# Performance work log

Measured on AMD Instinct MI355X. Metric: run time of the kernel, lower is better.

Reference implementation:

```python
import jax, jax.numpy as jnp
import numpy as np

N_NODES, IN_DIM, HID, LAT, N_EDGES = 50000, 3000, 512, 30, 800000
NEG_SLOPE = 0.2


def setup_inputs() -> dict:
    key = jax.random.key(0)
    ks = jax.random.split(key, 6)
    x = jax.random.normal(ks[0], (N_NODES, IN_DIM), dtype=jnp.float32)
    edge_index = jax.random.randint(ks[1], (2, N_EDGES), 0, N_NODES, dtype=jnp.int64)
    # xavier-normal-ish scales
    W1 = jax.random.normal(ks[2], (IN_DIM, HID), dtype=jnp.float32) * 0.02
    W2 = jax.random.normal(ks[3], (HID, LAT), dtype=jnp.float32) * 0.06
    att_src = jax.random.normal(ks[4], (HID,), dtype=jnp.float32) * 0.1
    att_dst = jax.random.normal(ks[5], (HID,), dtype=jnp.float32) * 0.1
    return {"x": x, "edge_index": edge_index, "W1": W1, "W2": W2,
            "att_src": att_src, "att_dst": att_dst}


def _segment_softmax(e, seg, num_segments):
    # numerically stable softmax over variable-degree dst neighborhoods
    m = jax.ops.segment_max(e, seg, num_segments=num_segments)
    m = jnp.where(jnp.isfinite(m), m, 0.0)  # empty segments -> 0, harmless
    p = jnp.exp(e - m[seg])
    s = jax.ops.segment_sum(p, seg, num_segments=num_segments)
    return p / (s[seg] + 1e-16)


def reference(x, edge_index, W1, W2, att_src, att_dst):
    N = x.shape[0]
    src, dst = edge_index[0], edge_index[1]  # messages flow src(j) -> dst(i)

    # ---- conv1: full GAT layer (heads=1, no self-loops, no bias) ----
    h1 = x @ W1                                   # [N, 512]
    a_src = h1 @ att_src                          # [N]
    a_dst = h1 @ att_dst                          # [N]
    e = jax.nn.leaky_relu(a_src[src] + a_dst[dst], NEG_SLOPE)  # [E]
    alpha = _segment_softmax(e, dst, N)           # [E] (also tied attn for conv3)
    agg1 = jax.ops.segment_sum(h1[src] * alpha[:, None], dst, num_segments=N)
    x1 = jax.nn.elu(agg1)                         # [N, 512]

    # ---- conv2: attention=False -> plain linear projection ----
    x2 = x1 @ W2                                  # [N, 30] (latent embedding)

    # ---- conv3: tied weights (W2^T) + tied attention from conv1 ----
    h3 = x2 @ W2.T                                # [N, 512]
    agg3 = jax.ops.segment_sum(h3[src] * alpha[:, None], dst, num_segments=N)
    x3 = jax.nn.elu(agg3)

    # ---- conv4: attention=False, tied weights (W1^T) ----
    x4 = x3 @ W1.T                                # [N, in_channels]
    return (x2, x4)
```

## Files before the change

kernel.cpp:

```cpp
#include <hip/hip_runtime.h>

#define N_NODES 50000
#define IN_DIM  3000
#define HID     512
#define LAT     30
#define N_EDGES 800000
#define M_PAD   50048
#define K1_PAD  3008
#define N4_PAD  3072

typedef __bf16 bf16;
typedef unsigned int uint;
typedef __attribute__((ext_vector_type(4))) float f32x4;
typedef __attribute__((ext_vector_type(8))) bf16 bf16x8;

__device__ __forceinline__ float bf2f(bf16 b){ return (float)b; }

__device__ __forceinline__ void gl16(const void* g, void* l){
  __builtin_amdgcn_global_load_lds(
      (const __attribute__((address_space(1))) void*)g,
      (__attribute__((address_space(3))) void*)l, 16, 0, 0);
}

__device__ __forceinline__ int xcd_swz(int orig, int nwg){
  int q = nwg >> 3, r = nwg & 7;
  int xcd = orig & 7, lid = orig >> 3;
  return (xcd < r ? xcd*(q+1) : r*(q+1) + (xcd-r)*q) + lid;
}

__global__ void k_w1t(const float* __restrict__ W1, bf16* __restrict__ W1T){
  int k = blockIdx.x*256 + threadIdx.x;
  int n = blockIdx.y;
  if (k >= K1_PAD) return;
  float v = (k < IN_DIM) ? W1[(long)k*HID + n] : 0.f;
  W1T[(long)n*K1_PAD + k] = (bf16)v;
}
__global__ void k_w1p(const float* __restrict__ W1, bf16* __restrict__ W1P){
  int k = blockIdx.x*256 + threadIdx.x;
  int n = blockIdx.y;
  if (k >= HID) return;
  float v = (n < IN_DIM) ? W1[(long)n*HID + k] : 0.f;
  W1P[(long)n*HID + k] = (bf16)v;
}
__global__ void k_w2t(const float* __restrict__ W2, bf16* __restrict__ W2T){
  int k = blockIdx.x*256 + threadIdx.x;
  int n = blockIdx.y;
  if (k >= HID) return;
  float v = (n < LAT) ? W2[(long)k*LAT + n] : 0.f;
  W2T[(long)n*HID + k] = (bf16)v;
}
__global__ void k_w2p(const float* __restrict__ W2, bf16* __restrict__ W2P){
  int t = blockIdx.x*256 + threadIdx.x;
  if (t >= HID*32) return;
  int n = t >> 5, k = t & 31;
  W2P[t] = (bf16)((k < LAT) ? W2[(long)n*LAT + k] : 0.f);
}

__global__ __launch_bounds__(256) void gemm_a32(
    const float* __restrict__ X, const bf16* __restrict__ Bw, bf16* __restrict__ C)
{
  __shared__ bf16 Alds[2][128*32];
  __shared__ bf16 Blds[2][128*32];
  const int NBX = HID/128;
  const int tid  = threadIdx.x;
  const int lane = tid & 63;
  const int w    = tid >> 6;
  const int wm   = (w >> 1) * 64, wn = (w & 1) * 64;
  const int wgid = xcd_swz(blockIdx.x, gridDim.x);
  const int col0 = (wgid % NBX) * 128, row0 = (wgid / NBX) * 128;
  const int Ksteps = K1_PAD/32;

  f32x4 acc[4][4];
  #pragma unroll
  for (int mi=0;mi<4;mi++)
    #pragma unroll
    for (int ni=0;ni<4;ni++)
      acc[mi][ni] = (f32x4){0.f,0.f,0.f,0.f};

  const int arow = tid >> 1;
  const int cg   = (tid & 1) * 16;
  const float* pA = X + (long)min(row0 + arow, N_NODES-1) * IN_DIM;

  const int sr = tid >> 2;
  const int sc = (tid & 3) * 16;
  const char* gB = (const char*)(Bw + (long)(col0 + sr) * K1_PAD) + sc;
  const long bstep = (long)64 * K1_PAD * 2;
  char* lB0 = (char*)&Blds[0][0] + sr*64 + sc;
  char* lB1 = (char*)&Blds[1][0] + sr*64 + sc;

  {
    int kb = cg;
    float4 q0 = *(const float4*)(pA + kb);
    float4 q1 = *(const float4*)(pA + kb + 4);
    float4 q2 = *(const float4*)(pA + kb + 8);
    float4 q3 = *(const float4*)(pA + kb + 12);
    gl16(gB, lB0);
    gl16(gB + bstep, lB0 + 64*64);
    bf16x8 v0, v1;
    v0[0]=(bf16)q0.x; v0[1]=(bf16)q0.y; v0[2]=(bf16)q0.z; v0[3]=(bf16)q0.w;
    v0[4]=(bf16)q1.x; v0[5]=(bf16)q1.y; v0[6]=(bf16)q1.z; v0[7]=(bf16)q1.w;
    v1[0]=(bf16)q2.x; v1[1]=(bf16)q2.y; v1[2]=(bf16)q2.z; v1[3]=(bf16)q2.w;
    v1[4]=(bf16)q3.x; v1[5]=(bf16)q3.y; v1[6]=(bf16)q3.z; v1[7]=(bf16)q3.w;
    *(bf16x8*)&Alds[0][arow*32 + cg]     = v0;
    *(bf16x8*)&Alds[0][arow*32 + cg + 8] = v1;
  }

  for (int ks = 0; ks < Ksteps; ks++){
    const int c = ks & 1;
    __syncthreads();
    const bool pf = (ks+1 < Ksteps);
    float4 q0,q1,q2,q3;
    if (pf){
      int kb = (ks+1)*32 + cg;
      q0 = *(const float4*)(pA + min(kb,      IN_DIM-4));
      q1 = *(const float4*)(pA + min(kb + 4,  IN_DIM-4));
      q2 = *(const float4*)(pA + min(kb + 8,  IN_DIM-4));
      q3 = *(const float4*)(pA + min(kb + 12, IN_DIM-4));
      const char* g = gB + (long)(ks+1)*64;
      char* l = c ? lB0 : lB1;
      gl16(g, l);
      gl16(g + bstep, l + 64*64);
    }
    bf16x8 af[4], bfr[4];
    #pragma unroll
    for (int mi=0;mi<4;mi++)
      af[mi] = *(const bf16x8*)&Alds[c][(wm + mi*16 + (lane & 15))*32 + (lane>>4)*8];
    #pragma unroll
    for (int ni=0;ni<4;ni++)
      bfr[ni] = *(const bf16x8*)&Blds[c][(wn + ni*16 + (lane & 15))*32 + (lane>>4)*8];
    #pragma unroll
    for (int mi=0;mi<4;mi++)
      #pragma unroll
      for (int ni=0;ni<4;ni++)
        acc[mi][ni] = __builtin_amdgcn_mfma_f32_16x16x32_bf16(af[mi], bfr[ni], acc[mi][ni], 0, 0, 0);
    if (pf){
      bf16x8 v0, v1;
      v0[0]=(bf16)q0.x; v0[1]=(bf16)q0.y; v0[2]=(bf16)q0.z; v0[3]=(bf16)q0.w;
      v0[4]=(bf16)q1.x; v0[5]=(bf16)q1.y; v0[6]=(bf16)q1.z; v0[7]=(bf16)q1.w;
      v1[0]=(bf16)q2.x; v1[1]=(bf16)q2.y; v1[2]=(bf16)q2.z; v1[3]=(bf16)q2.w;
      v1[4]=(bf16)q3.x; v1[5]=(bf16)q3.y; v1[6]=(bf16)q3.z; v1[7]=(bf16)q3.w;
      *(bf16x8*)&Alds[c^1][arow*32 + cg]     = v0;
      *(bf16x8*)&Alds[c^1][arow*32 + cg + 8] = v1;
    }
  }

  const int crb  = (lane >> 4) * 4;
  const int ccol = lane & 15;
  #pragma unroll
  for (int mi=0;mi<4;mi++){
    #pragma unroll
    for (int v=0;v<4;v++){
      int r = row0 + wm + mi*16 + crb + v;
      if (r >= N_NODES) continue;
      #pragma unroll
      for (int ni=0;ni<4;ni++){
        int cc = col0 + wn + ni*16 + ccol;
        C[(long)r*HID + cc] = (bf16)acc[mi][ni][v];
      }
    }
  }
}

template<bool C_F32, bool ELU>
__global__ __launch_bounds__(256) void gemm_glds(
    const bf16* __restrict__ A, const bf16* __restrict__ B, void* __restrict__ Cp,
    int lda, int ldb, int Ksteps, int Mvalid, int Nvalid, int ldc, int NBX)
{
  __shared__ bf16 Alds[128*32];
  __shared__ bf16 Blds[128*32];
  const int tid  = threadIdx.x;
  const int lane = tid & 63;
  const int w    = tid >> 6;
  const int wm   = (w >> 1) * 64, wn = (w & 1) * 64;
  const int wgid = xcd_swz(blockIdx.x, gridDim.x);
  const int col0 = (wgid % NBX) * 128, row0 = (wgid / NBX) * 128;

  f32x4 acc[4][4];
  #pragma unroll
  for (int mi=0;mi<4;mi++)
    #pragma unroll
    for (int ni=0;ni<4;ni++)
      acc[mi][ni] = (f32x4){0.f,0.f,0.f,0.f};

  const int sr = tid >> 2;
  const int sc = (tid & 3) * 16;

  const char* ga = (const char*)(A + (long)(row0 + sr) * lda) + sc;
  const char* gb = (const char*)(B + (long)(col0 + sr) * ldb) + sc;
  char* la = (char*)Alds + sr*64 + sc;
  char* lb = (char*)Blds + sr*64 + sc;
  const long astep = (long)64 * lda * 2;
  const long bstep = (long)64 * ldb * 2;

  for (int ks = 0; ks < Ksteps; ks++){
    const long ko = (long)ks * 64;
    gl16(ga + ko,         la);
    gl16(ga + ko + astep, la + 64*64);
    gl16(gb + ko,         lb);
    gl16(gb + ko + bstep, lb + 64*64);
    __syncthreads();

    bf16x8 af[4], bfr[4];
    #pragma unroll
    for (int mi=0;mi<4;mi++)
      af[mi] = *(const bf16x8*)&Alds[(wm + mi*16 + (lane & 15))*32 + (lane>>4)*8];
    #pragma unroll
    for (int ni=0;ni<4;ni++)
      bfr[ni] = *(const bf16x8*)&Blds[(wn + ni*16 + (lane & 15))*32 + (lane>>4)*8];
    #pragma unroll
    for (int mi=0;mi<4;mi++)
      #pragma unroll
      for (int ni=0;ni<4;ni++)
        acc[mi][ni] = __builtin_amdgcn_mfma_f32_16x16x32_bf16(af[mi], bfr[ni], acc[mi][ni], 0, 0, 0);
    __syncthreads();
  }

  const int crb  = (lane >> 4) * 4;
  const int ccol = lane & 15;
  #pragma unroll
  for (int mi=0;mi<4;mi++){
    #pragma unroll
    for (int v=0;v<4;v++){
      int r = row0 + wm + mi*16 + crb + v;
      if (r >= Mvalid) continue;
      #pragma unroll
      for (int ni=0;ni<4;ni++){
        int c = col0 + wn + ni*16 + ccol;
        if (c >= Nvalid) continue;
        float val = acc[mi][ni][v];
        if (ELU) val = (val > 0.f) ? val : expm1f(val);
        if (C_F32) ((float*)Cp)[(long)r*ldc + c] = val;
        else       ((bf16*)Cp)[(long)r*ldc + c] = (bf16)val;
      }
    }
  }
}

__global__ void k_attdots(const bf16* __restrict__ h1, const float* __restrict__ att_s,
                          const float* __restrict__ att_d, float* __restrict__ a_src,
                          float* __restrict__ a_dst){
  int gid = blockIdx.x * blockDim.x + threadIdx.x;
  int row = gid >> 6, lane = gid & 63;
  if (row >= N_NODES) return;
  bf16x8 hv = *(const bf16x8*)(h1 + (long)row*HID + lane*8);
  float s1 = 0.f, s2 = 0.f;
  #pragma unroll
  for (int j=0;j<8;j++){
    float h = bf2f(hv[j]);
    s1 = fmaf(h, att_s[lane*8+j], s1);
    s2 = fmaf(h, att_d[lane*8+j], s2);
  }
  #pragma unroll
  for (int o=32;o>0;o>>=1){ s1 += __shfl_down(s1,o); s2 += __shfl_down(s2,o); }
  if (lane == 0){ a_src[row] = s1; a_dst[row] = s2; }
}

__global__ void k_deg(const int* __restrict__ ei, int* __restrict__ deg){
  int e = blockIdx.x*256 + threadIdx.x;
  if (e >= N_EDGES) return;
  atomicAdd(&deg[ei[N_EDGES + e]], 1);
}

__global__ void k_scan(const int* __restrict__ deg, int* __restrict__ off, int* __restrict__ cur){
  const int n = M_PAD, T = 1024;
  int t = threadIdx.x;
  const int per = (n + T - 1) / T;
  int s0 = t*per, s1 = min(n, s0+per);
  int sum = 0;
  for (int i=s0;i<s1;i++) sum += deg[i];
  __shared__ int sd[1024];
  sd[t] = sum; __syncthreads();
  for (int o=1;o<T;o<<=1){
    int x = (t>=o) ? sd[t-o] : 0;
    __syncthreads();
    sd[t] += x;
    __syncthreads();
  }
  int run = sd[t] - sum;
  for (int i=s0;i<s1;i++){
    off[i] = run; cur[i] = run;
    run += deg[i];
  }
  if (s0 < n && s1 == n) off[n] = run;
}

__global__ void k_fill(const int* __restrict__ ei, int* __restrict__ cur,
                       int* __restrict__ csr_src, const float* __restrict__ a_s,
                       const float* __restrict__ a_d, float* __restrict__ p_e){
  int e = blockIdx.x*256 + threadIdx.x;
  if (e >= N_EDGES) return;
  int s = ei[e];
  int d = ei[N_EDGES + e];
  int pos = atomicAdd(&cur[d], 1);
  csr_src[pos] = s;
  float v = a_s[s] + a_d[d];
  v = (v > 0.f) ? v : 0.2f*v;
  p_e[pos] = __expf(v);
}

__global__ __launch_bounds__(512) void k_agg1(
    const int* __restrict__ off, const int* __restrict__ csr_src,
    const float* __restrict__ p_edge,
    const bf16* __restrict__ h1, bf16* __restrict__ x1,
    float* __restrict__ s_node)
{
  const int i = blockIdx.x;
  const int t = threadIdx.x;
  const int start = off[i];
  const int deg = off[i+1] - start;
  __shared__ float p_sh[512];
  __shared__ int   s_sh[512];

  float acc = 0.f, ssum = 0.f;
  for (int base=0; base<deg; base+=512){
    int cnt = min(512, deg-base);
    if (t < cnt){
      p_sh[t] = p_edge[start+base+t];
      s_sh[t] = csr_src[start+base+t];
    }
    __syncthreads();
    for (int k=0;k<cnt;k++){
      float pk = p_sh[k];
      ssum += pk;
      acc = fmaf(pk, bf2f(h1[(long)s_sh[k]*HID + t]), acc);
    }
    __syncthreads();
  }
  float val = acc / (ssum + 1e-16f);
  val = (val > 0.f) ? val : expm1f(val);
  x1[(long)i*HID + t] = (bf16)val;
  if (t == 0) s_node[i] = ssum;
}

__global__ void k_agg3(const int* __restrict__ off, const int* __restrict__ csr_src,
                       const float* __restrict__ p_edge, const float* __restrict__ s_node,
                       const float* __restrict__ x2, bf16* __restrict__ aggb)
{
  int i = blockIdx.x*8 + (threadIdx.x >> 5);
  int lane = threadIdx.x & 31;
  if (i >= M_PAD) return;
  float acc = 0.f;
  if (i < N_NODES){
    int s0 = off[i], d = off[i+1] - s0;
    for (int k=0;k<d;k++){
      int s = csr_src[s0+k];
      float pk = p_edge[s0+k];
      if (lane < LAT) acc = fmaf(pk, x2[(long)s*LAT + lane], acc);
    }
    acc *= 1.f/(s_node[i] + 1e-16f);
  }
  aggb[(long)i*32 + lane] = (bf16)((lane < LAT) ? acc : 0.f);
}

extern "C" void kernel_launch(void* const* d_in, const int* in_sizes, int n_in,
                              void* d_out, int out_size, void* d_ws, size_t ws_size,
                              hipStream_t stream)
{
  const float* x     = (const float*)d_in[0];
  const int*   ei    = (const int*)d_in[1];
  const float* W1    = (const float*)d_in[2];
  const float* W2    = (const float*)d_in[3];
  const float* att_s = (const float*)d_in[4];
  const float* att_d = (const float*)d_in[5];

  float* out_x2 = (float*)d_out;
  float* out_x4 = (float*)d_out + (long)N_NODES*LAT;

  bf16* h1 = (bf16*)out_x4;
  bf16* x1 = h1 + (long)M_PAD*HID;

  char* w = (char*)d_ws;
  bf16* W1T = (bf16*)w;  w += (long)HID*K1_PAD*2;
  bf16* W1P = (bf16*)w;  w += (long)N4_PAD*HID*2;
  bf16* W2T = (bf16*)w;  w += (long)128*HID*2;
  bf16* W2P = (bf16*)w;  w += (long)HID*32*2;
  bf16* x3  = (bf16*)w;  w += (long)M_PAD*HID*2;
  bf16* aggb= (bf16*)w;  w += (long)M_PAD*32*2;
  int* deg  = (int*)w;   w += (long)M_PAD*4;
  int* offs = (int*)w;   w += (long)(M_PAD+64)*4;
  int* cur  = (int*)w;   w += (long)M_PAD*4;
  int* csr  = (int*)w;   w += (long)N_EDGES*4;
  float* p_e = (float*)w; w += (long)N_EDGES*4;
  float* s_n = (float*)w; w += (long)M_PAD*4;
  float* a_s = (float*)w; w += (long)M_PAD*4;
  float* a_d = (float*)w; w += (long)M_PAD*4;

  k_w1t<<<dim3((K1_PAD+255)/256, HID), 256, 0, stream>>>(W1, W1T);
  k_w1p<<<dim3((HID+255)/256, N4_PAD), 256, 0, stream>>>(W1, W1P);
  k_w2t<<<dim3(2, 128), 256, 0, stream>>>(W2, W2T);
  k_w2p<<<(HID*32+255)/256, 256, 0, stream>>>(W2, W2P);

  hipMemsetAsync(deg, 0, (size_t)M_PAD*4, stream);
  k_deg<<<(N_EDGES+255)/256, 256, 0, stream>>>(ei, deg);
  k_scan<<<1, 1024, 0, stream>>>(deg, offs, cur);

  gemm_a32<<<(M_PAD/128)*(HID/128), 256, 0, stream>>>(x, W1T, h1);

  k_attdots<<<(N_NODES*64)/256, 256, 0, stream>>>(h1, att_s, att_d, a_s, a_d);

  k_fill<<<(N_EDGES+255)/256, 256, 0, stream>>>(ei, cur, csr, a_s, a_d, p_e);

  k_agg1<<<N_NODES, 512, 0, stream>>>(offs, csr, p_e, h1, x1, s_n);

  gemm_glds<true,false><<<1*(M_PAD/128), 256, 0, stream>>>(
      x1, W2T, out_x2, HID, HID, HID/32, N_NODES, LAT, LAT, 1);

  k_agg3<<<(M_PAD+7)/8, 256, 0, stream>>>(offs, csr, p_e, s_n, out_x2, aggb);
  gemm_glds<false,true><<<(HID/128)*(M_PAD/128), 256, 0, stream>>>(
      aggb, W2P, x3, 32, 32, 1, M_PAD, HID, HID, HID/128);

  gemm_glds<true,false><<<(N4_PAD/128)*(M_PAD/128), 256, 0, stream>>>(
      x3, W1P, out_x4, HID, HID, HID/32, N_NODES, IN_DIM, IN_DIM, N4_PAD/128);
}
```

Measured before the change: 1.362 ms.

## Load GEMM A operand directly into MFMA registers, dropping LDS staging for X

The first GEMM (x @ W1) now has each lane load its fp32 X fragments from global memory straight into registers in MFMA layout and convert to bf16 in place, instead of staging A through LDS. B still goes through double-buffered global_load_lds, with manual vmcnt waits and barriers, in a two-deep register/LDS pipeline unrolled by two. The aim is to remove LDS traffic and a sync for A and to keep more loads in flight. The cost is uncoalesced, strided 32-byte row reads of X duplicated across the two column-half waves, plus higher register pressure under launch_bounds(256,2).

```diff
diff --git a/kernel.cpp b/kernel.cpp
--- a/kernel.cpp
+++ b/kernel.cpp
@@ -28,6 +28,13 @@
   return (xcd < r ? xcd*(q+1) : r*(q+1) + (xcd-r)*q) + lid;
 }
 
+__device__ __forceinline__ bf16x8 cvt8(float4 a, float4 b){
+  bf16x8 r;
+  r[0]=(bf16)a.x; r[1]=(bf16)a.y; r[2]=(bf16)a.z; r[3]=(bf16)a.w;
+  r[4]=(bf16)b.x; r[5]=(bf16)b.y; r[6]=(bf16)b.z; r[7]=(bf16)b.w;
+  return r;
+}
+
 __global__ void k_w1t(const float* __restrict__ W1, bf16* __restrict__ W1T){
   int k = blockIdx.x*256 + threadIdx.x;
   int n = blockIdx.y;
@@ -56,10 +63,50 @@
   W2P[t] = (bf16)((k < LAT) ? W2[(long)n*LAT + k] : 0.f);
 }
 
-__global__ __launch_bounds__(256) void gemm_a32(
+
+#define STAGE_M(kc, P0,P1,P2,P3,P4,P5,P6,P7, LB) do{                            \
+  int k_ = (kc)*32 + klane;                                                     \
+  int ka_ = min(k_, IN_DIM-4), kb_ = min(k_+4, IN_DIM-4);                       \
+  P0 = *(const float4*)(X + off0 + ka_); P1 = *(const float4*)(X + off0 + kb_); \
+  P2 = *(const float4*)(X + off1 + ka_); P3 = *(const float4*)(X + off1 + kb_); \
+  P4 = *(const float4*)(X + off2 + ka_); P5 = *(const float4*)(X + off2 + kb_); \
+  P6 = *(const float4*)(X + off3 + ka_); P7 = *(const float4*)(X + off3 + kb_); \
+  gl16(gB + (long)(kc)*64, LB);                                                 \
+  gl16(gB + (long)(kc)*64 + bstep, LB + 64*64);                                 \
+}while(0)
+
+#define COMPUTE_M(P0,P1,P2,P3,P4,P5,P6,P7, LBASE) do{                           \
+  asm volatile("s_waitcnt vmcnt(10)" ::: "memory");                             \
+  __builtin_amdgcn_s_barrier();                                                 \
+  bf16x8 af0 = cvt8(P0,P1), af1 = cvt8(P2,P3);                                  \
+  bf16x8 af2 = cvt8(P4,P5), af3 = cvt8(P6,P7);                                  \
+  const bf16* Lb_ = (LBASE);                                                    \
+  bf16x8 bf0 = *(const bf16x8*)&Lb_[(wn +  0 + r_l)*32 + klane];                \
+  bf16x8 bf1 = *(const bf16x8*)&Lb_[(wn + 16 + r_l)*32 + klane];                \
+  bf16x8 bf2 = *(const bf16x8*)&Lb_[(wn + 32 + r_l)*32 + klane];                \
+  bf16x8 bf3 = *(const bf16x8*)&Lb_[(wn + 48 + r_l)*32 + klane];                \
+  acc[0][0] = __builtin_amdgcn_mfma_f32_16x16x32_bf16(af0, bf0, acc[0][0],0,0,0); \
+  acc[0][1] = __builtin_amdgcn_mfma_f32_16x16x32_bf16(af0, bf1, acc[0][1],0,0,0); \
+  acc[0][2] = __builtin_amdgcn_mfma_f32_16x16x32_bf16(af0, bf2, acc[0][2],0,0,0); \
+  acc[0][3] = __builtin_amdgcn_mfma_f32_16x16x32_bf16(af0, bf3, acc[0][3],0,0,0); \
+  acc[1][0] = __builtin_amdgcn_mfma_f32_16x16x32_bf16(af1, bf0, acc[1][0],0,0,0); \
+  acc[1][1] = __builtin_amdgcn_mfma_f32_16x16x32_bf16(af1, bf1, acc[1][1],0,0,0); \
+  acc[1][2] = __builtin_amdgcn_mfma_f32_16x16x32_bf16(af1, bf2, acc[1][2],0,0,0); \
+  acc[1][3] = __builtin_amdgcn_mfma_f32_16x16x32_bf16(af1, bf3, acc[1][3],0,0,0); \
+  acc[2][0] = __builtin_amdgcn_mfma_f32_16x16x32_bf16(af2, bf0, acc[2][0],0,0,0); \
+  acc[2][1] = __builtin_amdgcn_mfma_f32_16x16x32_bf16(af2, bf1, acc[2][1],0,0,0); \
+  acc[2][2] = __builtin_amdgcn_mfma_f32_16x16x32_bf16(af2, bf2, acc[2][2],0,0,0); \
+  acc[2][3] = __builtin_amdgcn_mfma_f32_16x16x32_bf16(af2, bf3, acc[2][3],0,0,0); \
+  acc[3][0] = __builtin_amdgcn_mfma_f32_16x16x32_bf16(af3, bf0, acc[3][0],0,0,0); \
+  acc[3][1] = __builtin_amdgcn_mfma_f32_16x16x32_bf16(af3, bf1, acc[3][1],0,0,0); \
+  acc[3][2] = __builtin_amdgcn_mfma_f32_16x16x32_bf16(af3, bf2, acc[3][2],0,0,0); \
+  acc[3][3] = __builtin_amdgcn_mfma_f32_16x16x32_bf16(af3, bf3, acc[3][3],0,0,0); \
+  __builtin_amdgcn_s_barrier();                                                 \
+}while(0)
+
+__global__ __launch_bounds__(256, 2) void gemm_a32r(
     const float* __restrict__ X, const bf16* __restrict__ Bw, bf16* __restrict__ C)
 {
-  __shared__ bf16 Alds[2][128*32];
   __shared__ bf16 Blds[2][128*32];
   const int NBX = HID/128;
   const int tid  = threadIdx.x;
@@ -68,7 +115,6 @@
   const int wm   = (w >> 1) * 64, wn = (w & 1) * 64;
   const int wgid = xcd_swz(blockIdx.x, gridDim.x);
   const int col0 = (wgid % NBX) * 128, row0 = (wgid / NBX) * 128;
-  const int Ksteps = K1_PAD/32;
 
   f32x4 acc[4][4];
   #pragma unroll
@@ -77,71 +123,31 @@
     for (int ni=0;ni<4;ni++)
       acc[mi][ni] = (f32x4){0.f,0.f,0.f,0.f};
 
-  const int arow = tid >> 1;
-  const int cg   = (tid & 1) * 16;
-  const float* pA = X + (long)min(row0 + arow, N_NODES-1) * IN_DIM;
+  const int klane = (lane >> 4) * 8;
+  const int r_l   = lane & 15;
+  const int off0 = min(row0 + wm +  0 + r_l, N_NODES-1) * IN_DIM;
+  const int off1 = min(row0 + wm + 16 + r_l, N_NODES-1) * IN_DIM;
+  const int off2 = min(row0 + wm + 32 + r_l, N_NODES-1) * IN_DIM;
+  const int off3 = min(row0 + wm + 48 + r_l, N_NODES-1) * IN_DIM;
 
   const int sr = tid >> 2;
   const int sc = (tid & 3) * 16;
   const char* gB = (const char*)(Bw + (long)(col0 + sr) * K1_PAD) + sc;
   const long bstep = (long)64 * K1_PAD * 2;
-  char* lB0 = (char*)&Blds[0][0] + sr*64 + sc;
-  char* lB1 = (char*)&Blds[1][0] + sr*64 + sc;
-
-  {
-    int kb = cg;
-    float4 q0 = *(const float4*)(pA + kb);
-    float4 q1 = *(const float4*)(pA + kb + 4);
-    float4 q2 = *(const float4*)(pA + kb + 8);
-    float4 q3 = *(const float4*)(pA + kb + 12);
-    gl16(gB, lB0);
-    gl16(gB + bstep, lB0 + 64*64);
-    bf16x8 v0, v1;
-    v0[0]=(bf16)q0.x; v0[1]=(bf16)q0.y; v0[2]=(bf16)q0.z; v0[3]=(bf16)q0.w;
-    v0[4]=(bf16)q1.x; v0[5]=(bf16)q1.y; v0[6]=(bf16)q1.z; v0[7]=(bf16)q1.w;
-    v1[0]=(bf16)q2.x; v1[1]=(bf16)q2.y; v1[2]=(bf16)q2.z; v1[3]=(bf16)q2.w;
-    v1[4]=(bf16)q3.x; v1[5]=(bf16)q3.y; v1[6]=(bf16)q3.z; v1[7]=(bf16)q3.w;
-    *(bf16x8*)&Alds[0][arow*32 + cg]     = v0;
-    *(bf16x8*)&Alds[0][arow*32 + cg + 8] = v1;
-  }
-
-  for (int ks = 0; ks < Ksteps; ks++){
-    const int c = ks & 1;
-    __syncthreads();
-    const bool pf = (ks+1 < Ksteps);
-    float4 q0,q1,q2,q3;
-    if (pf){
-      int kb = (ks+1)*32 + cg;
-      q0 = *(const float4*)(pA + min(kb,      IN_DIM-4));
-      q1 = *(const float4*)(pA + min(kb + 4,  IN_DIM-4));
-      q2 = *(const float4*)(pA + min(kb + 8,  IN_DIM-4));
-      q3 = *(const float4*)(pA + min(kb + 12, IN_DIM-4));
-      const char* g = gB + (long)(ks+1)*64;
-      char* l = c ? lB0 : lB1;
-      gl16(g, l);
-      gl16(g + bstep, l + 64*64);
-    }
-    bf16x8 af[4], bfr[4];
-    #pragma unroll
-    for (int mi=0;mi<4;mi++)
-      af[mi] = *(const bf16x8*)&Alds[c][(wm + mi*16 + (lane & 15))*32 + (lane>>4)*8];
-    #pragma unroll
-    for (int ni=0;ni<4;ni++)
-      bfr[ni] = *(const bf16x8*)&Blds[c][(wn + ni*16 + (lane & 15))*32 + (lane>>4)*8];
-    #pragma unroll
-    for (int mi=0;mi<4;mi++)
-      #pragma unroll
-      for (int ni=0;ni<4;ni++)
-        acc[mi][ni] = __builtin_amdgcn_mfma_f32_16x16x32_bf16(af[mi], bfr[ni], acc[mi][ni], 0, 0, 0);
-    if (pf){
-      bf16x8 v0, v1;
-      v0[0]=(bf16)q0.x; v0[1]=(bf16)q0.y; v0[2]=(bf16)q0.z; v0[3]=(bf16)q0.w;
-      v0[4]=(bf16)q1.x; v0[5]=(bf16)q1.y; v0[6]=(bf16)q1.z; v0[7]=(bf16)q1.w;
-      v1[0]=(bf16)q2.x; v1[1]=(bf16)q2.y; v1[2]=(bf16)q2.z; v1[3]=(bf16)q2.w;
-      v1[4]=(bf16)q3.x; v1[5]=(bf16)q3.y; v1[6]=(bf16)q3.z; v1[7]=(bf16)q3.w;
-      *(bf16x8*)&Alds[c^1][arow*32 + cg]     = v0;
-      *(bf16x8*)&Alds[c^1][arow*32 + cg + 8] = v1;
-    }
+  char* lB0w = (char*)&Blds[0][0] + sr*64 + sc;
+  char* lB1w = (char*)&Blds[1][0] + sr*64 + sc;
+
+  float4 a00,a01,a02,a03,a04,a05,a06,a07;
+  float4 a10,a11,a12,a13,a14,a15,a16,a17;
+
+  STAGE_M(0, a00,a01,a02,a03,a04,a05,a06,a07, lB0w);
+  STAGE_M(1, a10,a11,a12,a13,a14,a15,a16,a17, lB1w);
+
+  for (int kb = 0; kb < 94; kb += 2){
+    COMPUTE_M(a00,a01,a02,a03,a04,a05,a06,a07, &Blds[0][0]);
+    STAGE_M(min(kb+2,93), a00,a01,a02,a03,a04,a05,a06,a07, lB0w);
+    COMPUTE_M(a10,a11,a12,a13,a14,a15,a16,a17, &Blds[1][0]);
+    STAGE_M(min(kb+3,93), a10,a11,a12,a13,a14,a15,a16,a17, lB1w);
   }
 
   const int crb  = (lane >> 4) * 4;
@@ -394,7 +400,7 @@
   k_deg<<<(N_EDGES+255)/256, 256, 0, stream>>>(ei, deg);
   k_scan<<<1, 1024, 0, stream>>>(deg, offs, cur);
 
-  gemm_a32<<<(M_PAD/128)*(HID/128), 256, 0, stream>>>(x, W1T, h1);
+  gemm_a32r<<<(M_PAD/128)*(HID/128), 256, 0, stream>>>(x, W1T, h1);
 
   k_attdots<<<(N_NODES*64)/256, 256, 0, stream>>>(h1, att_s, att_d, a_s, a_d);
 
```

New measurement: 1.435 ms. 5.3% more time.

## Stream fp32 X tiles directly into LDS and convert to bf16 on read

Applied to the files above, without the earlier changes.

The X@W1 GEMM now loads fp32 A tiles straight into shared memory with global_load_lds, using an XOR-swizzled layout. Each A fragment is converted to bf16 when it is read from LDS, rather than being loaded into registers, converted, and stored. This removes the register staging, the manual prefetch and the register pressure of the old path. The price is that the double buffer becomes a single buffer with two barriers per K step, so global loads and MFMA work inside a block no longer overlap. The A LDS footprint doubles, and the conversion is repeated by both column-half waves.

```diff
diff --git a/kernel.cpp b/kernel.cpp
--- a/kernel.cpp
+++ b/kernel.cpp
@@ -28,6 +28,13 @@
   return (xcd < r ? xcd*(q+1) : r*(q+1) + (xcd-r)*q) + lid;
 }
 
+__device__ __forceinline__ bf16x8 cvt8v(f32x4 a, f32x4 b){
+  bf16x8 r;
+  r[0]=(bf16)a[0]; r[1]=(bf16)a[1]; r[2]=(bf16)a[2]; r[3]=(bf16)a[3];
+  r[4]=(bf16)b[0]; r[5]=(bf16)b[1]; r[6]=(bf16)b[2]; r[7]=(bf16)b[3];
+  return r;
+}
+
 __global__ void k_w1t(const float* __restrict__ W1, bf16* __restrict__ W1T){
   int k = blockIdx.x*256 + threadIdx.x;
   int n = blockIdx.y;
@@ -56,11 +63,11 @@
   W2P[t] = (bf16)((k < LAT) ? W2[(long)n*LAT + k] : 0.f);
 }
 
-__global__ __launch_bounds__(256) void gemm_a32(
+__global__ __launch_bounds__(256) void gemm_xw1(
     const float* __restrict__ X, const bf16* __restrict__ Bw, bf16* __restrict__ C)
 {
-  __shared__ bf16 Alds[2][128*32];
-  __shared__ bf16 Blds[2][128*32];
+  __shared__ float Af[128*32];
+  __shared__ bf16  Bl[128*32];
   const int NBX = HID/128;
   const int tid  = threadIdx.x;
   const int lane = tid & 63;
@@ -68,7 +75,6 @@
   const int wm   = (w >> 1) * 64, wn = (w & 1) * 64;
   const int wgid = xcd_swz(blockIdx.x, gridDim.x);
   const int col0 = (wgid % NBX) * 128, row0 = (wgid / NBX) * 128;
-  const int Ksteps = K1_PAD/32;
 
   f32x4 acc[4][4];
   #pragma unroll
@@ -77,71 +83,49 @@
     for (int ni=0;ni<4;ni++)
       acc[mi][ni] = (f32x4){0.f,0.f,0.f,0.f};
 
-  const int arow = tid >> 1;
-  const int cg   = (tid & 1) * 16;
-  const float* pA = X + (long)min(row0 + arow, N_NODES-1) * IN_DIM;
+  const int ar  = tid >> 3;
+  const int apc = tid & 7;
+  const int ac4 = (apc ^ (ar & 7)) * 4;
+  int aoff[4];
+  #pragma unroll
+  for (int i=0;i<4;i++)
+    aoff[i] = min(row0 + i*32 + ar, N_NODES-1) * IN_DIM;
 
   const int sr = tid >> 2;
   const int sc = (tid & 3) * 16;
   const char* gB = (const char*)(Bw + (long)(col0 + sr) * K1_PAD) + sc;
   const long bstep = (long)64 * K1_PAD * 2;
-  char* lB0 = (char*)&Blds[0][0] + sr*64 + sc;
-  char* lB1 = (char*)&Blds[1][0] + sr*64 + sc;
-
-  {
-    int kb = cg;
-    float4 q0 = *(const float4*)(pA + kb);
-    float4 q1 = *(const float4*)(pA + kb + 4);
-    float4 q2 = *(const float4*)(pA + kb + 8);
-    float4 q3 = *(const float4*)(pA + kb + 12);
-    gl16(gB, lB0);
-    gl16(gB + bstep, lB0 + 64*64);
-    bf16x8 v0, v1;
-    v0[0]=(bf16)q0.x; v0[1]=(bf16)q0.y; v0[2]=(bf16)q0.z; v0[3]=(bf16)q0.w;
-    v0[4]=(bf16)q1.x; v0[5]=(bf16)q1.y; v0[6]=(bf16)q1.z; v0[7]=(bf16)q1.w;
-    v1[0]=(bf16)q2.x; v1[1]=(bf16)q2.y; v1[2]=(bf16)q2.z; v1[3]=(bf16)q2.w;
-    v1[4]=(bf16)q3.x; v1[5]=(bf16)q3.y; v1[6]=(bf16)q3.z; v1[7]=(bf16)q3.w;
-    *(bf16x8*)&Alds[0][arow*32 + cg]     = v0;
-    *(bf16x8*)&Alds[0][arow*32 + cg + 8] = v1;
-  }
-
-  for (int ks = 0; ks < Ksteps; ks++){
-    const int c = ks & 1;
-    __syncthreads();
-    const bool pf = (ks+1 < Ksteps);
-    float4 q0,q1,q2,q3;
-    if (pf){
-      int kb = (ks+1)*32 + cg;
-      q0 = *(const float4*)(pA + min(kb,      IN_DIM-4));
-      q1 = *(const float4*)(pA + min(kb + 4,  IN_DIM-4));
-      q2 = *(const float4*)(pA + min(kb + 8,  IN_DIM-4));
-      q3 = *(const float4*)(pA + min(kb + 12, IN_DIM-4));
-      const char* g = gB + (long)(ks+1)*64;
-      char* l = c ? lB0 : lB1;
-      gl16(g, l);
-      gl16(g + bstep, l + 64*64);
-    }
+  float* lA = Af + tid*4;
+  char*  lB = (char*)Bl + sr*64 + sc;
+
+  for (int ks = 0; ks < 94; ks++){
+    int kcl = min(ks*32 + ac4, IN_DIM-4);
+    #pragma unroll
+    for (int i=0;i<4;i++)
+      gl16(X + aoff[i] + kcl, lA + i*1024);
+    gl16(gB + (long)ks*64,         lB);
+    gl16(gB + (long)ks*64 + bstep, lB + 64*64);
+    __syncthreads();
+
+    const int g2 = (lane >> 4) * 2;
     bf16x8 af[4], bfr[4];
     #pragma unroll
-    for (int mi=0;mi<4;mi++)
-      af[mi] = *(const bf16x8*)&Alds[c][(wm + mi*16 + (lane & 15))*32 + (lane>>4)*8];
+    for (int mi=0;mi<4;mi++){
+      int row = wm + mi*16 + (lane & 15);
+      int rx  = row & 7;
+      f32x4 f0 = *(const f32x4*)&Af[row*32 + ((g2    ) ^ rx)*4];
+      f32x4 f1 = *(const f32x4*)&Af[row*32 + ((g2 + 1) ^ rx)*4];
+      af[mi] = cvt8v(f0, f1);
+    }
     #pragma unroll
     for (int ni=0;ni<4;ni++)
-      bfr[ni] = *(const bf16x8*)&Blds[c][(wn + ni*16 + (lane & 15))*32 + (lane>>4)*8];
+      bfr[ni] = *(const bf16x8*)&Bl[(wn + ni*16 + (lane & 15))*32 + (lane>>4)*8];
     #pragma unroll
     for (int mi=0;mi<4;mi++)
       #pragma unroll
       for (int ni=0;ni<4;ni++)
         acc[mi][ni] = __builtin_amdgcn_mfma_f32_16x16x32_bf16(af[mi], bfr[ni], acc[mi][ni], 0, 0, 0);
-    if (pf){
-      bf16x8 v0, v1;
-      v0[0]=(bf16)q0.x; v0[1]=(bf16)q0.y; v0[2]=(bf16)q0.z; v0[3]=(bf16)q0.w;
-      v0[4]=(bf16)q1.x; v0[5]=(bf16)q1.y; v0[6]=(bf16)q1.z; v0[7]=(bf16)q1.w;
-      v1[0]=(bf16)q2.x; v1[1]=(bf16)q2.y; v1[2]=(bf16)q2.z; v1[3]=(bf16)q2.w;
-      v1[4]=(bf16)q3.x; v1[5]=(bf16)q3.y; v1[6]=(bf16)q3.z; v1[7]=(bf16)q3.w;
-      *(bf16x8*)&Alds[c^1][arow*32 + cg]     = v0;
-      *(bf16x8*)&Alds[c^1][arow*32 + cg + 8] = v1;
-    }
+    __syncthreads();
   }
 
   const int crb  = (lane >> 4) * 4;
@@ -394,7 +378,7 @@
   k_deg<<<(N_EDGES+255)/256, 256, 0, stream>>>(ei, deg);
   k_scan<<<1, 1024, 0, stream>>>(deg, offs, cur);
 
-  gemm_a32<<<(M_PAD/128)*(HID/128), 256, 0, stream>>>(x, W1T, h1);
+  gemm_xw1<<<(M_PAD/128)*(HID/128), 256, 0, stream>>>(x, W1T, h1);
 
   k_attdots<<<(N_NODES*64)/256, 256, 0, stream>>>(h1, att_s, att_d, a_s, a_d);
 
```

Result: faster. 1.217 ms (-10.7%).
